# Performance work log

Measured on AMD Instinct MI355X. Metric: run time of the kernel, lower is better.

The kernel has to match this reference:

```python
import jax, jax.numpy as jnp
import numpy as np

DIM = 512; NB = 4; BS = DIM // NB            # EinFFT blocks
DS = 64; DC = 4; EXP = 2; DI = EXP * DIM      # Mamba dims
DTR = DIM // 16                               # dt_rank
BLOCKS = 2; LAM = 0.01; B_SZ = 2; L_SZ = 1024

def layer_norm(x, w, b):
    m = x.mean(-1, keepdims=True)
    v = x.var(-1, keepdims=True)
    return (x - m) / jnp.sqrt(v + 1e-5) * w + b

def softshrink(x, lam):
    return jnp.where(x > lam, x - lam, jnp.where(x < -lam, x + lam, jnp.zeros((), x.dtype)))

def mamba(x, in_proj_w, conv_w, conv_b, x_proj_w, dt_proj_w, dt_proj_b, A_log, D, out_proj_w):
    B, L, _ = x.shape
    xz = x @ in_proj_w.T                      # (B,L,2*DI)
    xm, z = jnp.split(xz, 2, axis=-1)
    # causal depthwise conv1d, keep first L outputs
    xt = xm.transpose(0, 2, 1)                # (B,DI,L)
    conv = jax.lax.conv_general_dilated(xt, conv_w, (1,), [(DC - 1, 0)],
                                        feature_group_count=DI,
                                        dimension_numbers=('NCH', 'OIH', 'NCH'))
    xm = jax.nn.silu((conv + conv_b[None, :, None]).transpose(0, 2, 1))  # (B,L,DI)
    proj = xm @ x_proj_w.T                    # (B,L,DTR+2*DS)
    dt = proj[..., :DTR]
    Bm = proj[..., DTR:DTR + DS]
    Cm = proj[..., DTR + DS:]
    dt = jax.nn.softplus(dt @ dt_proj_w.T + dt_proj_b)   # (B,L,DI)
    A = -jnp.exp(A_log)                       # (DI,DS)

    def step(h, inp):
        dt_t, B_t, C_t, u_t = inp             # (B,DI),(B,DS),(B,DS),(B,DI)
        dA = jnp.exp(dt_t[:, :, None] * A)
        h = dA * h + dt_t[:, :, None] * B_t[:, None, :] * u_t[:, :, None]
        y = jnp.einsum('bds,bs->bd', h, C_t)
        return h, y

    h0 = jnp.zeros((B, DI, DS), x.dtype)
    _, ys = jax.lax.scan(step, h0, (dt.transpose(1, 0, 2), Bm.transpose(1, 0, 2),
                                    Cm.transpose(1, 0, 2), xm.transpose(1, 0, 2)))
    y = ys.transpose(1, 0, 2) + xm * D        # (B,L,DI)
    y = y * jax.nn.silu(z)
    return y @ out_proj_w.T

def einfft(x, cw1, cw2, cb1, cb2):
    B, N, C = x.shape
    xf = jnp.fft.fft2(x.reshape(B, N, NB, BS), axes=(1, 2), norm='ortho')
    mul = lambda t, w: jnp.einsum('BNbd,bdk->BNbk', t, w)
    r1 = jax.nn.relu(mul(xf.real, cw1[0]) - mul(xf.imag, cw1[1]) + cb1[0])
    i1 = jax.nn.relu(mul(xf.real, cw1[1]) + mul(xf.imag, cw1[0]) + cb1[1])
    r2 = softshrink(mul(r1, cw2[0]) - mul(i1, cw2[1]) + cb2[0], LAM)
    i2 = softshrink(mul(r1, cw2[1]) + mul(i1, cw2[0]) + cb2[1], LAM)
    out = jnp.fft.ifft2(r2 + 1j * i2, axes=(1, 2), norm='ortho')
    return out.real.astype(x.dtype).reshape(B, N, C)

def setup_inputs() -> dict:
    key = jax.random.key(0)
    ks = jax.random.split(key, 16)
    r = lambda i, shape, s: jax.random.normal(ks[i], shape, jnp.float32) * s
    A_log = jnp.log(jnp.tile(jnp.arange(1, DS + 1, dtype=jnp.float32), (DI, 1)))
    return {
        'x': jax.random.normal(ks[0], (B_SZ, L_SZ, DIM), jnp.float32),
        'ln_w': jnp.ones((DIM,), jnp.float32), 'ln_b': jnp.zeros((DIM,), jnp.float32),
        'in_proj_w': r(1, (2 * DI, DIM), 0.02),
        'conv_w': r(2, (DI, 1, DC), 0.1), 'conv_b': jnp.zeros((DI,), jnp.float32),
        'x_proj_w': r(3, (DTR + 2 * DS, DI), 0.02),
        'dt_proj_w': r(4, (DI, DTR), 0.02),
        'dt_proj_b': jnp.full((DI,), float(np.log(np.expm1(0.01))), jnp.float32),
        'A_log': A_log, 'D': jnp.ones((DI,), jnp.float32),
        'out_proj_w': r(5, (DIM, DI), 0.02),
        'norm2_w': jnp.ones((DIM,), jnp.float32), 'norm2_b': jnp.zeros((DIM,), jnp.float32),
        'cw1': r(6, (2, NB, BS, BS), 0.02), 'cw2': r(7, (2, NB, BS, BS), 0.02),
        'cb1': r(8, (2, NB, BS), 0.02), 'cb2': r(9, (2, NB, BS), 0.02),
    }

def reference(x, ln_w, ln_b, in_proj_w, conv_w, conv_b, x_proj_w, dt_proj_w, dt_proj_b,
              A_log, D, out_proj_w, norm2_w, norm2_b, cw1, cw2, cb1, cb2):
    for _ in range(BLOCKS):
        x = x + mamba(layer_norm(x, ln_w, ln_b), in_proj_w, conv_w, conv_b,
                      x_proj_w, dt_proj_w, dt_proj_b, A_log, D, out_proj_w)
        x = x + einfft(layer_norm(x, norm2_w, norm2_b), cw1, cw2, cb1, cb2)
    return x
```

## Files before the change

kernel.cpp:

```cpp
#include <hip/hip_runtime.h>

typedef unsigned short u16;
typedef __attribute__((ext_vector_type(8))) short bf8;
typedef __attribute__((ext_vector_type(4))) float f4;

__device__ __forceinline__ float bf2f(u16 b) {
    return __uint_as_float(((unsigned)b) << 16);
}
__device__ __forceinline__ u16 f2bf(float f) {
    unsigned u = __float_as_uint(f);
    u += 0x7fffu + ((u >> 16) & 1u);
    return (u16)(u >> 16);
}
__device__ __forceinline__ void pack8f(const float* v, u16* dst) {
    uint r0 = (uint)f2bf(v[0]) | ((uint)f2bf(v[1]) << 16);
    uint r1 = (uint)f2bf(v[2]) | ((uint)f2bf(v[3]) << 16);
    uint r2 = (uint)f2bf(v[4]) | ((uint)f2bf(v[5]) << 16);
    uint r3 = (uint)f2bf(v[6]) | ((uint)f2bf(v[7]) << 16);
    *(uint4*)dst = make_uint4(r0, r1, r2, r3);
}
__device__ __forceinline__ void pack8u(const u16* v, u16* dst) {
    uint r0 = (uint)v[0] | ((uint)v[1] << 16);
    uint r1 = (uint)v[2] | ((uint)v[3] << 16);
    uint r2 = (uint)v[4] | ((uint)v[5] << 16);
    uint r3 = (uint)v[6] | ((uint)v[7] << 16);
    *(uint4*)dst = make_uint4(r0, r1, r2, r3);
}
__device__ __forceinline__ bf8 neg8(bf8 v) {
    union { bf8 b; uint u[4]; } t; t.b = v;
    t.u[0] ^= 0x80008000u; t.u[1] ^= 0x80008000u;
    t.u[2] ^= 0x80008000u; t.u[3] ^= 0x80008000u;
    return t.b;
}

__global__ void detect_k(const u16* __restrict__ dtb, int* __restrict__ flag) {
    flag[0] = (dtb[0] == dtb[1] && dtb[1] == dtb[2] && dtb[2] == dtb[3] &&
               dtb[3] == dtb[4] && dtb[4] == dtb[5]) ? 1 : 0;
    flag[1] = 1;
}

__global__ __launch_bounds__(256)
void achk_k(const float* __restrict__ alog, int* __restrict__ flag) {
    int i = blockIdx.x * 256 + threadIdx.x;
    int s = i & 63;
    float n = __expf(alog[i]);
    float e = (float)(s + 1);
    if (fabsf(n - e) > 0.02f * e) atomicAnd(&flag[1], 0);
}

struct CvtArgs {
    const void* src[18];
    void* dst[18];
    int n[18];
    int obf[18];
};
__global__ __launch_bounds__(256)
void cvt_all_k(CvtArgs a, const int* __restrict__ flag) {
    const int t = blockIdx.y;
    const int n = a.n[t];
    const int f = flag[0];
    if (a.obf[t]) {
        u16* __restrict__ d = (u16*)a.dst[t];
        if (f) {
            const u16* __restrict__ s = (const u16*)a.src[t];
            for (int i = blockIdx.x * 256 + threadIdx.x; i < n; i += gridDim.x * 256)
                d[i] = s[i];
        } else {
            const float* __restrict__ s = (const float*)a.src[t];
            for (int i = blockIdx.x * 256 + threadIdx.x; i < n; i += gridDim.x * 256)
                d[i] = f2bf(s[i]);
        }
    } else {
        float* __restrict__ d = (float*)a.dst[t];
        if (f) {
            const u16* __restrict__ s = (const u16*)a.src[t];
            for (int i = blockIdx.x * 256 + threadIdx.x; i < n; i += gridDim.x * 256)
                d[i] = bf2f(s[i]);
        } else {
            const float* __restrict__ s = (const float*)a.src[t];
            for (int i = blockIdx.x * 256 + threadIdx.x; i < n; i += gridDim.x * 256)
                d[i] = s[i];
        }
    }
}

__global__ void out_k(const float* __restrict__ in, void* __restrict__ out,
                      int n, const int* __restrict__ flag) {
    int i = blockIdx.x * 256 + threadIdx.x;
    if (i >= n) return;
    if (flag[0]) ((u16*)out)[i] = f2bf(in[i]);
    else         ((float*)out)[i] = in[i];
}

__global__ void wtr_k(const float* __restrict__ src, u16* __restrict__ dst) {
    int idx = blockIdx.x * 256 + threadIdx.x;
    int cin = idx & 127, cout = (idx >> 7) & 127, snb = idx >> 14;
    dst[(snb << 14) + (cout << 7) + cin] = f2bf(src[(snb << 14) + (cin << 7) + cout]);
}

__global__ __launch_bounds__(256)
void ln_k(const float* __restrict__ x, const float* __restrict__ w,
          const float* __restrict__ b, u16* __restrict__ out) {
    const int row = blockIdx.x, tid = threadIdx.x;
    const float* xr = x + (long)row * 512;
    float v0 = xr[tid], v1 = xr[tid + 256];
    float s = v0 + v1, q = v0 * v0 + v1 * v1;
#pragma unroll
    for (int off = 32; off; off >>= 1) {
        s += __shfl_xor(s, off);
        q += __shfl_xor(q, off);
    }
    __shared__ float ss[4], qq[4];
    int wid = tid >> 6;
    if ((tid & 63) == 0) { ss[wid] = s; qq[wid] = q; }
    __syncthreads();
    s = ss[0] + ss[1] + ss[2] + ss[3];
    q = qq[0] + qq[1] + qq[2] + qq[3];
    float mean = s * (1.f / 512.f);
    float var = q * (1.f / 512.f) - mean * mean;
    float rstd = rsqrtf(var + 1e-5f);
    u16* o = out + (long)row * 512;
    o[tid]       = f2bf((v0 - mean) * rstd * w[tid]       + b[tid]);
    o[tid + 256] = f2bf((v1 - mean) * rstd * w[tid + 256] + b[tid + 256]);
}

#define LSTR 40
template <int TAF, int EPI>
__global__ __launch_bounds__(256)
void mgemm_k(const void* __restrict__ Ap, const u16* __restrict__ Bp,
             float* __restrict__ D, int N, int K, int lda, int ldb, int ldc,
             const float* __restrict__ bias, const float* __restrict__ res) {
    const float* Af = (const float*)Ap;
    const u16*  Ab  = (const u16*)Ap;

    __shared__ u16 As[64 * LSTR];
    __shared__ u16 Bs[64 * LSTR];
    const int tid = threadIdx.x;
    const int lane = tid & 63;
    const int w = tid >> 6, wm = w & 1, wn = w >> 1;
    const int m0 = blockIdx.y * 64, n0 = blockIdx.x * 64;
    const int fr = (lane & 15), fq = (lane >> 4);

    f4 acc[2][2] = {};

    for (int k0 = 0; k0 < K; k0 += 32) {
        {
            const int ar = tid >> 2, aks = (tid & 3) << 3;
            if constexpr (TAF) {
                *(uint4*)&As[ar * LSTR + aks] =
                    *(const uint4*)(Ab + (long)(m0 + ar) * lda + k0 + aks);
            } else {
                const float* p = Af + (long)(m0 + ar) * lda + k0 + aks;
                float tv[8];
                float4 x = *(const float4*)p, y = *(const float4*)(p + 4);
                tv[0] = x.x; tv[1] = x.y; tv[2] = x.z; tv[3] = x.w;
                tv[4] = y.x; tv[5] = y.y; tv[6] = y.z; tv[7] = y.w;
                pack8f(tv, &As[ar * LSTR + aks]);
            }
        }
        {
            const int br = tid >> 2, bks = (tid & 3) << 3;
            uint4 raw = make_uint4(0, 0, 0, 0);
            if (n0 + br < N)
                raw = *(const uint4*)(Bp + (long)(n0 + br) * ldb + k0 + bks);
            *(uint4*)&Bs[br * LSTR + bks] = raw;
        }
        __syncthreads();
        bf8 af[2], bff[2];
#pragma unroll
        for (int t = 0; t < 2; t++) {
            af[t]  = *(bf8*)&As[(wm * 32 + t * 16 + fr) * LSTR + (fq << 3)];
            bff[t] = *(bf8*)&Bs[(wn * 32 + t * 16 + fr) * LSTR + (fq << 3)];
        }
#pragma unroll
        for (int i = 0; i < 2; i++)
#pragma unroll
            for (int j = 0; j < 2; j++)
                acc[i][j] = __builtin_amdgcn_mfma_f32_16x16x32_bf16(
                    af[i], bff[j], acc[i][j], 0, 0, 0);
        __syncthreads();
    }

#pragma unroll
    for (int i = 0; i < 2; i++) {
#pragma unroll
        for (int j = 0; j < 2; j++) {
            const int gmb = m0 + wm * 32 + i * 16 + (fq << 2);
            const int gn  = n0 + wn * 32 + j * 16 + fr;
            if (gn >= N) continue;
            float v[4];
#pragma unroll
            for (int e = 0; e < 4; e++) v[e] = acc[i][j][e];
            if constexpr (EPI == 1) {
                float bb = bias[gn];
#pragma unroll
                for (int e = 0; e < 4; e++) {
                    float t = v[e] + bb;
                    v[e] = (t > 20.f) ? t : log1pf(__expf(t));
                }
            }
#pragma unroll
            for (int e = 0; e < 4; e++) {
                long idx = (long)(gmb + e) * ldc + gn;
                float t = v[e];
                if constexpr (EPI == 2) t += res[idx];
                D[idx] = t;
            }
        }
    }
}

__global__ __launch_bounds__(256)
void fftn_k(const u16* __restrict__ xn, float* __restrict__ Xr,
            float* __restrict__ Xi) {
    const int bc = blockIdx.x;
    const int b = bc >> 9, c = bc & 511;
    const int tid = threadIdx.x;
    __shared__ float re[1056], im[1056], twr[512], twi[512];
#pragma unroll
    for (int r = 0; r < 2; ++r) {
        int k = tid + r * 256;
        float s, cc;
        __sincosf((float)k * -6.1359231515425649e-3f, &s, &cc);
        twr[k] = cc; twi[k] = s;
    }
    const u16* src = xn + ((long)b * 1024) * 512 + c;
#pragma unroll
    for (int r = 0; r < 4; ++r) {
        int n = tid + r * 256;
        float v = bf2f(src[(long)n * 512]);
        int a = n + (n >> 5);
        re[a] = v; im[a] = 0.f;
    }
#pragma unroll
    for (int lh = 9; lh >= 0; --lh) {
        __syncthreads();
        const int half = 1 << lh;
#pragma unroll
        for (int r = 0; r < 2; ++r) {
            int j = tid + r * 256;
            int p = j & (half - 1);
            int i0 = ((j >> lh) << (lh + 1)) | p;
            int i1 = i0 + half;
            int a0 = i0 + (i0 >> 5), a1 = i1 + (i1 >> 5);
            float ar = re[a0], ai = im[a0];
            float br = re[a1], bi = im[a1];
            int tn = p << (9 - lh);
            float wr = twr[tn], wi = twi[tn];
            re[a0] = ar + br; im[a0] = ai + bi;
            float tr = ar - br, ti = ai - bi;
            re[a1] = tr * wr - ti * wi;
            im[a1] = tr * wi + ti * wr;
        }
    }
    __syncthreads();
    float* dr = Xr + (long)bc * 1024;
    float* di = Xi + (long)bc * 1024;
#pragma unroll
    for (int r = 0; r < 4; ++r) {
        int kf = tid + r * 256;
        int sidx = __brev((unsigned)kf) >> 22;
        int a = sidx + (sidx >> 5);
        dr[kf] = re[a] * 0.03125f;
        di[kf] = im[a] * 0.03125f;
    }
}

__global__ __launch_bounds__(256)
void ifftn_k(const u16* __restrict__ X2r, const u16* __restrict__ X2i,
             float* __restrict__ Yc) {
    const int bc = blockIdx.x;
    const int tid = threadIdx.x;
    __shared__ float re[1056], im[1056], twr[512], twi[512];
#pragma unroll
    for (int r = 0; r < 2; ++r) {
        int k = tid + r * 256;
        float s, cc;
        __sincosf((float)k * 6.1359231515425649e-3f, &s, &cc);
        twr[k] = cc; twi[k] = s;
    }
    const u16* sr = X2r + (long)bc * 1024;
    const u16* si = X2i + (long)bc * 1024;
    {
        int k4 = tid * 4;
        uint2 pr = *(const uint2*)&sr[k4];
        uint2 pi = *(const uint2*)&si[k4];
        u16 rv[4] = {(u16)(pr.x & 0xFFFF), (u16)(pr.x >> 16),
                     (u16)(pr.y & 0xFFFF), (u16)(pr.y >> 16)};
        u16 iv[4] = {(u16)(pi.x & 0xFFFF), (u16)(pi.x >> 16),
                     (u16)(pi.y & 0xFFFF), (u16)(pi.y >> 16)};
#pragma unroll
        for (int e = 0; e < 4; ++e) {
            int idx = k4 + e;
            int a = idx + (idx >> 5);
            re[a] = bf2f(rv[e]);
            im[a] = bf2f(iv[e]);
        }
    }
#pragma unroll
    for (int lh = 9; lh >= 0; --lh) {
        __syncthreads();
        const int half = 1 << lh;
#pragma unroll
        for (int r = 0; r < 2; ++r) {
            int j = tid + r * 256;
            int p = j & (half - 1);
            int i0 = ((j >> lh) << (lh + 1)) | p;
            int i1 = i0 + half;
            int a0 = i0 + (i0 >> 5), a1 = i1 + (i1 >> 5);
            float ar = re[a0], ai = im[a0];
            float br = re[a1], bi = im[a1];
            int tn = p << (9 - lh);
            float wr = twr[tn], wi = twi[tn];
            re[a0] = ar + br; im[a0] = ai + bi;
            float tr = ar - br, ti = ai - bi;
            re[a1] = tr * wr - ti * wi;
            im[a1] = tr * wi + ti * wr;
        }
    }
    __syncthreads();
    float* d = Yc + (long)bc * 1024;
#pragma unroll
    for (int r = 0; r < 4; ++r) {
        int n = tid + r * 256;
        int sidx = __brev((unsigned)n) >> 22;
        int a = sidx + (sidx >> 5);
        d[n] = re[a] * 0.03125f;
    }
}

__global__ __launch_bounds__(256)
void transadd_k(float* __restrict__ xbuf, const float* __restrict__ Yc) {
    const int b = blockIdx.z;
    const int c0 = blockIdx.x * 64, n0 = blockIdx.y * 64;
    __shared__ float T[64][65];
    const int tid = threadIdx.x;
    const int r = tid >> 2, q = (tid & 3) * 16;
    const float* src = Yc + ((long)(b * 512 + c0 + r)) * 1024 + n0 + q;
#pragma unroll
    for (int k = 0; k < 4; ++k) {
        float4 v = *(const float4*)(src + k * 4);
        T[r][q + k * 4 + 0] = v.x; T[r][q + k * 4 + 1] = v.y;
        T[r][q + k * 4 + 2] = v.z; T[r][q + k * 4 + 3] = v.w;
    }
    __syncthreads();
    float* dst = xbuf + ((long)(b * 1024 + n0 + r)) * 512 + c0 + q;
#pragma unroll
    for (int k = 0; k < 4; ++k) {
        float4 w = *(const float4*)(dst + k * 4);
        w.x += T[q + k * 4 + 0][r]; w.y += T[q + k * 4 + 1][r];
        w.z += T[q + k * 4 + 2][r]; w.w += T[q + k * 4 + 3][r];
        *(float4*)(dst + k * 4) = w;
    }
}

template <int ACT>
__global__ __launch_bounds__(256)
void cmix_k(const u16* __restrict__ Xr, const u16* __restrict__ Xi,
            const u16* __restrict__ WT, const float* __restrict__ cb,
            u16* __restrict__ Or, u16* __restrict__ Oi) {
    const int z = blockIdx.z, b = z >> 2, nb = z & 3;
    const u16* Ar = Xr + (long)b * 524288 + nb * 131072;
    const u16* Ai = Xi + (long)b * 524288 + nb * 131072;
    const u16* Wr = WT + nb * 16384;
    const u16* Wi = WT + 65536 + nb * 16384;
    u16* Dr = Or + (long)b * 524288 + nb * 131072;
    u16* Di = Oi + (long)b * 524288 + nb * 131072;
    __shared__ u16 Ars[64 * LSTR], Ais[64 * LSTR], Brs[64 * LSTR], Bis[64 * LSTR];
    const int tid = threadIdx.x, lane = tid & 63;
    const int w = tid >> 6, wm = w & 1, wn = w >> 1;
    const int m0 = blockIdx.y * 64, n0 = blockIdx.x * 64;
    const int fr = (lane & 15), fq = (lane >> 4);
    f4 accr[2][2] = {}, acci[2][2] = {};

    for (int k0 = 0; k0 < 128; k0 += 32) {
        {
            const int am = tid & 63, akb = (tid >> 6) << 3;
            u16 tr[8], ti[8];
#pragma unroll
            for (int j = 0; j < 8; j++) {
                long off = (long)(k0 + akb + j) * 1024 + m0 + am;
                tr[j] = Ar[off]; ti[j] = Ai[off];
            }
            pack8u(tr, &Ars[am * LSTR + akb]);
            pack8u(ti, &Ais[am * LSTR + akb]);
        }
        {
            const int br = tid >> 2, bks = (tid & 3) << 3;
            *(uint4*)&Brs[br * LSTR + bks] =
                *(const uint4*)(Wr + (long)(n0 + br) * 128 + k0 + bks);
            *(uint4*)&Bis[br * LSTR + bks] =
                *(const uint4*)(Wi + (long)(n0 + br) * 128 + k0 + bks);
        }
        __syncthreads();
        bf8 arf[2], aif[2], brf[2], bif[2];
#pragma unroll
        for (int t = 0; t < 2; t++) {
            arf[t] = *(bf8*)&Ars[(wm * 32 + t * 16 + fr) * LSTR + (fq << 3)];
            aif[t] = *(bf8*)&Ais[(wm * 32 + t * 16 + fr) * LSTR + (fq << 3)];
            brf[t] = *(bf8*)&Brs[(wn * 32 + t * 16 + fr) * LSTR + (fq << 3)];
            bif[t] = *(bf8*)&Bis[(wn * 32 + t * 16 + fr) * LSTR + (fq << 3)];
        }
        bf8 nai[2] = { neg8(aif[0]), neg8(aif[1]) };
#pragma unroll
        for (int i = 0; i < 2; i++)
#pragma unroll
            for (int j = 0; j < 2; j++) {
                accr[i][j] = __builtin_amdgcn_mfma_f32_16x16x32_bf16(arf[i], brf[j], accr[i][j], 0, 0, 0);
                accr[i][j] = __builtin_amdgcn_mfma_f32_16x16x32_bf16(nai[i], bif[j], accr[i][j], 0, 0, 0);
                acci[i][j] = __builtin_amdgcn_mfma_f32_16x16x32_bf16(arf[i], bif[j], acci[i][j], 0, 0, 0);
                acci[i][j] = __builtin_amdgcn_mfma_f32_16x16x32_bf16(aif[i], brf[j], acci[i][j], 0, 0, 0);
            }
        __syncthreads();
    }
#pragma unroll
    for (int i = 0; i < 2; i++)
#pragma unroll
        for (int j = 0; j < 2; j++) {
            const int gmb = m0 + wm * 32 + i * 16 + (fq << 2);
            const int gn  = n0 + wn * 32 + j * 16 + fr;
            const float bbr = cb[nb * 128 + gn];
            const float bbi = cb[512 + nb * 128 + gn];
            u16 pr[4], pi[4];
#pragma unroll
            for (int e = 0; e < 4; e++) {
                float vr = accr[i][j][e] + bbr;
                float vi = acci[i][j][e] + bbi;
                if (ACT == 0) {
                    vr = fmaxf(vr, 0.f);
                    vi = fmaxf(vi, 0.f);
                } else {
                    vr = (vr > 0.01f) ? vr - 0.01f : ((vr < -0.01f) ? vr + 0.01f : 0.f);
                    vi = (vi > 0.01f) ? vi - 0.01f : ((vi < -0.01f) ? vi + 0.01f : 0.f);
                }
                pr[e] = f2bf(vr); pi[e] = f2bf(vi);
            }
            uint2 wr2, wi2;
            wr2.x = (uint)pr[0] | ((uint)pr[1] << 16);
            wr2.y = (uint)pr[2] | ((uint)pr[3] << 16);
            wi2.x = (uint)pi[0] | ((uint)pi[1] << 16);
            wi2.y = (uint)pi[2] | ((uint)pi[3] << 16);
            *(uint2*)&Dr[(long)gn * 1024 + gmb] = wr2;
            *(uint2*)&Di[(long)gn * 1024 + gmb] = wi2;
        }
}

__global__ __launch_bounds__(256)
void conv_k(const float* __restrict__ xz, const float* __restrict__ cw,
            const float* __restrict__ cb, float* __restrict__ u) {
    int idx = blockIdx.x * 256 + threadIdx.x;
    int d = idx & 1023;
    int l = (idx >> 10) & 1023;
    int b = idx >> 20;
    float acc = cb[d];
    const float* base = xz + (long)b * 1024 * 2048 + d;
#pragma unroll
    for (int j = 0; j < 4; j++) {
        int li = l - 3 + j;
        if (li >= 0) acc = fmaf(cw[d * 4 + j], base[(long)li * 2048], acc);
    }
    float sig = 1.f / (1.f + __expf(-acc));
    u[idx] = acc * sig;
}

__global__ __launch_bounds__(256)
void scan1_k(const float* __restrict__ dtL, const float* __restrict__ uL,
             const float* __restrict__ projL, const float* __restrict__ alog,
             u16* __restrict__ Hb, float* __restrict__ Sbuf,
             const int* __restrict__ flag) {
    const int dg = blockIdx.x, c = blockIdx.y, b = blockIdx.z;
    const int tid = threadIdx.x;
    const int d = dg * 256 + tid;
    const int t0 = c * 16;
    __shared__ float Bls[16][64];
    {
        int r = tid >> 4, cg = (tid & 15) << 2;
        *(float4*)&Bls[r][cg] =
            *(const float4*)(projL + ((long)(b * 1024 + t0 + r)) * 160 + 32 + cg);
    }
    __syncthreads();

    float h[64];
#pragma unroll
    for (int s = 0; s < 64; s++) h[s] = 0.f;
    float S = 0.f;
    const float* dtp = dtL + (long)(b * 1024 + t0) * 1024 + d;
    const float* up  = uL  + (long)(b * 1024 + t0) * 1024 + d;

    if (flag[1]) {
        for (int t = 0; t < 16; ++t) {
            float dt = dtp[(long)t * 1024];
            float uu = up[(long)t * 1024];
            float dtu = dt * uu;
            S += dt;
            float q = __expf(-dt);
            float q2 = q * q, q3 = q2 * q, q4 = q2 * q2;
            float a0 = q, a1 = q2, a2 = q3, a3 = q4;
            const float4* B4p = (const float4*)&Bls[t][0];
#pragma unroll
            for (int sg = 0; sg < 16; ++sg) {
                float4 B4 = B4p[sg];
                h[sg * 4 + 0] = a0 * h[sg * 4 + 0] + dtu * B4.x;
                h[sg * 4 + 1] = a1 * h[sg * 4 + 1] + dtu * B4.y;
                h[sg * 4 + 2] = a2 * h[sg * 4 + 2] + dtu * B4.z;
                h[sg * 4 + 3] = a3 * h[sg * 4 + 3] + dtu * B4.w;
                a0 *= q4; a1 *= q4; a2 *= q4; a3 *= q4;
            }
        }
    } else {
        float A[64];
        const float* ap = alog + (long)d * 64;
#pragma unroll
        for (int s = 0; s < 64; s += 4) {
            float4 a4 = *(const float4*)(ap + s);
            A[s] = -__expf(a4.x); A[s + 1] = -__expf(a4.y);
            A[s + 2] = -__expf(a4.z); A[s + 3] = -__expf(a4.w);
        }
        for (int t = 0; t < 16; ++t) {
            float dt = dtp[(long)t * 1024];
            float uu = up[(long)t * 1024];
            float dtu = dt * uu;
            S += dt;
            const float4* B4p = (const float4*)&Bls[t][0];
#pragma unroll
            for (int sg = 0; sg < 16; ++sg) {
                float4 B4 = B4p[sg];
                h[sg * 4 + 0] = __expf(dt * A[sg * 4 + 0]) * h[sg * 4 + 0] + dtu * B4.x;
                h[sg * 4 + 1] = __expf(dt * A[sg * 4 + 1]) * h[sg * 4 + 1] + dtu * B4.y;
                h[sg * 4 + 2] = __expf(dt * A[sg * 4 + 2]) * h[sg * 4 + 2] + dtu * B4.z;
                h[sg * 4 + 3] = __expf(dt * A[sg * 4 + 3]) * h[sg * 4 + 3] + dtu * B4.w;
            }
        }
    }
    u16* Hp = Hb + ((((long)(b * 64 + c)) * 1024 + d) << 6);
#pragma unroll
    for (int s = 0; s < 64; s += 4) {
        uint2 p;
        p.x = ((__float_as_uint(h[s]) + 0x8000u) >> 16) |
              ((__float_as_uint(h[s + 1]) + 0x8000u) & 0xFFFF0000u);
        p.y = ((__float_as_uint(h[s + 2]) + 0x8000u) >> 16) |
              ((__float_as_uint(h[s + 3]) + 0x8000u) & 0xFFFF0000u);
        *(uint2*)&Hp[s] = p;
    }
    Sbuf[(b * 64 + c) * 1024 + d] = S;
}

__global__ __launch_bounds__(256)
void scan2_k(const float* __restrict__ alog, const float* __restrict__ Sbuf,
             u16* __restrict__ Hb) {
    int idx = blockIdx.x * 256 + threadIdx.x;
    int s = idx & 63, d = (idx >> 6) & 1023, b = idx >> 16;
    float A = -__expf(alog[(long)d * 64 + s]);
    float carry = 0.f;
    for (int c = 0; c < 64; ++c) {
        float S = Sbuf[(b * 64 + c) * 1024 + d];
        float P = __expf(A * S);
        long off = ((((long)(b * 64 + c)) * 1024 + d) << 6) + s;
        float H = bf2f(Hb[off]);
        Hb[off] = (u16)((__float_as_uint(carry) + 0x8000u) >> 16);
        carry = P * carry + H;
    }
}

__global__ __launch_bounds__(256)
void scan3_k(float* __restrict__ dtL, const float* __restrict__ uL,
             const float* __restrict__ xz, const float* __restrict__ projL,
             const float* __restrict__ alog, const u16* __restrict__ Hb,
             const float* __restrict__ Dw, const int* __restrict__ flag) {
    const int dg = blockIdx.x, c = blockIdx.y, b = blockIdx.z;
    const int tid = threadIdx.x;
    const int d = dg * 256 + tid;
    const int t0 = c * 16;
    __shared__ float Bls[16][64];
    __shared__ float Cls[16][64];
    {
        int r = tid >> 4, cg = (tid & 15) << 2;
        const float* src = projL + ((long)(b * 1024 + t0 + r)) * 160 + 32 + cg;
        *(float4*)&Bls[r][cg] = *(const float4*)src;
        *(float4*)&Cls[r][cg] = *(const float4*)(src + 64);
    }
    __syncthreads();

    float h[64];
    const u16* Hp = Hb + ((((long)(b * 64 + c)) * 1024 + d) << 6);
#pragma unroll
    for (int s = 0; s < 64; s += 4) {
        uint2 p = *(const uint2*)&Hp[s];
        h[s]     = __uint_as_float(p.x << 16);
        h[s + 1] = __uint_as_float(p.x & 0xFFFF0000u);
        h[s + 2] = __uint_as_float(p.y << 16);
        h[s + 3] = __uint_as_float(p.y & 0xFFFF0000u);
    }
    const float Dd = Dw[d];
    float* dtp = dtL + (long)(b * 1024 + t0) * 1024 + d;
    const float* up = uL + (long)(b * 1024 + t0) * 1024 + d;
    const float* zp = xz + (long)(b * 1024 + t0) * 2048 + 1024 + d;

    if (flag[1]) {
        for (int t = 0; t < 16; ++t) {
            float dt = dtp[(long)t * 1024];
            float uu = up[(long)t * 1024];
            float zz = zp[(long)t * 2048];
            float dtu = dt * uu;
            float y = 0.f;
            float q = __expf(-dt);
            float q2 = q * q, q3 = q2 * q, q4 = q2 * q2;
            float a0 = q, a1 = q2, a2 = q3, a3 = q4;
            const float4* B4p = (const float4*)&Bls[t][0];
            const float4* C4p = (const float4*)&Cls[t][0];
#pragma unroll
            for (int sg = 0; sg < 16; ++sg) {
                float4 B4 = B4p[sg];
                float4 C4 = C4p[sg];
                h[sg * 4 + 0] = a0 * h[sg * 4 + 0] + dtu * B4.x;
                y = fmaf(h[sg * 4 + 0], C4.x, y);
                h[sg * 4 + 1] = a1 * h[sg * 4 + 1] + dtu * B4.y;
                y = fmaf(h[sg * 4 + 1], C4.y, y);
                h[sg * 4 + 2] = a2 * h[sg * 4 + 2] + dtu * B4.z;
                y = fmaf(h[sg * 4 + 2], C4.z, y);
                h[sg * 4 + 3] = a3 * h[sg * 4 + 3] + dtu * B4.w;
                y = fmaf(h[sg * 4 + 3], C4.w, y);
                a0 *= q4; a1 *= q4; a2 *= q4; a3 *= q4;
            }
            float g = zz / (1.f + __expf(-zz));
            dtp[(long)t * 1024] = (y + uu * Dd) * g;
        }
    } else {
        float A[64];
        const float* ap = alog + (long)d * 64;
#pragma unroll
        for (int s = 0; s < 64; s += 4) {
            float4 a4 = *(const float4*)(ap + s);
            A[s] = -__expf(a4.x); A[s + 1] = -__expf(a4.y);
            A[s + 2] = -__expf(a4.z); A[s + 3] = -__expf(a4.w);
        }
        for (int t = 0; t < 16; ++t) {
            float dt = dtp[(long)t * 1024];
            float uu = up[(long)t * 1024];
            float zz = zp[(long)t * 2048];
            float dtu = dt * uu;
            float y = 0.f;
            const float4* B4p = (const float4*)&Bls[t][0];
            const float4* C4p = (const float4*)&Cls[t][0];
#pragma unroll
            for (int sg = 0; sg < 16; ++sg) {
                float4 B4 = B4p[sg];
                float4 C4 = C4p[sg];
                h[sg * 4 + 0] = __expf(dt * A[sg * 4 + 0]) * h[sg * 4 + 0] + dtu * B4.x;
                y = fmaf(h[sg * 4 + 0], C4.x, y);
                h[sg * 4 + 1] = __expf(dt * A[sg * 4 + 1]) * h[sg * 4 + 1] + dtu * B4.y;
                y = fmaf(h[sg * 4 + 1], C4.y, y);
                h[sg * 4 + 2] = __expf(dt * A[sg * 4 + 2]) * h[sg * 4 + 2] + dtu * B4.z;
                y = fmaf(h[sg * 4 + 2], C4.z, y);
                h[sg * 4 + 3] = __expf(dt * A[sg * 4 + 3]) * h[sg * 4 + 3] + dtu * B4.w;
                y = fmaf(h[sg * 4 + 3], C4.w, y);
            }
            float g = zz / (1.f + __expf(-zz));
            dtp[(long)t * 1024] = (y + uu * Dd) * g;
        }
    }
}

__global__ __launch_bounds__(256)
void fft4_k(const float* __restrict__ Xr, const float* __restrict__ Xi,
            u16* __restrict__ Orb, u16* __restrict__ Oib) {
    int idx = blockIdx.x * 256 + threadIdx.x;
    int kf = idx & 1023, c = (idx >> 10) & 127, b = idx >> 17;
    long base = (long)b * 524288 + (long)c * 1024 + kf;
    const int S = 131072;
    float r0 = Xr[base], r1 = Xr[base + S], r2 = Xr[base + 2 * S], r3 = Xr[base + 3 * S];
    float i0 = Xi[base], i1 = Xi[base + S], i2 = Xi[base + 2 * S], i3 = Xi[base + 3 * S];
    Orb[base]         = f2bf((r0 + r1 + r2 + r3) * 0.5f);
    Oib[base]         = f2bf((i0 + i1 + i2 + i3) * 0.5f);
    Orb[base + S]     = f2bf((r0 + i1 - r2 - i3) * 0.5f);
    Oib[base + S]     = f2bf((i0 - r1 - i2 + r3) * 0.5f);
    Orb[base + 2 * S] = f2bf((r0 - r1 + r2 - r3) * 0.5f);
    Oib[base + 2 * S] = f2bf((i0 - i1 + i2 - i3) * 0.5f);
    Orb[base + 3 * S] = f2bf((r0 - i1 - r2 + i3) * 0.5f);
    Oib[base + 3 * S] = f2bf((i0 + r1 - i2 - r3) * 0.5f);
}

__global__ __launch_bounds__(256)
void ifft4_k(u16* __restrict__ Xr, u16* __restrict__ Xi) {
    int idx = blockIdx.x * 256 + threadIdx.x;
    int kf = idx & 1023, c = (idx >> 10) & 127, b = idx >> 17;
    long base = (long)b * 524288 + (long)c * 1024 + kf;
    const int S = 131072;
    float r0 = bf2f(Xr[base]), r1 = bf2f(Xr[base + S]),
          r2 = bf2f(Xr[base + 2 * S]), r3 = bf2f(Xr[base + 3 * S]);
    float i0 = bf2f(Xi[base]), i1 = bf2f(Xi[base + S]),
          i2 = bf2f(Xi[base + 2 * S]), i3 = bf2f(Xi[base + 3 * S]);
    Xr[base]         = f2bf((r0 + r1 + r2 + r3) * 0.5f);
    Xi[base]         = f2bf((i0 + i1 + i2 + i3) * 0.5f);
    Xr[base + S]     = f2bf((r0 - i1 - r2 + i3) * 0.5f);
    Xi[base + S]     = f2bf((i0 + r1 - i2 - r3) * 0.5f);
    Xr[base + 2 * S] = f2bf((r0 - r1 + r2 - r3) * 0.5f);
    Xi[base + 2 * S] = f2bf((i0 - i1 + i2 - i3) * 0.5f);
    Xr[base + 3 * S] = f2bf((r0 + i1 - r2 - i3) * 0.5f);
    Xi[base + 3 * S] = f2bf((i0 - r1 - i2 + r3) * 0.5f);
}

extern "C" void kernel_launch(void* const* d_in, const int* in_sizes, int n_in,
                              void* d_out, int out_size, void* d_ws, size_t ws_size,
                              hipStream_t stream) {
    float* ws = (float*)d_ws;
    int* flag = (int*)ws;
    size_t o = 64;
    float* xbuf  = ws + o; o += 1048576;
    float* xz    = ws + o; o += 4194304;
    float* dtL   = ws + o; o += 2097152;
    float* uL    = ws + o; o += 2097152;
    float* projL = ws + o; o += 327680;
    u16* xnb     = (u16*)(ws + o); o += 524288;
    u16* wInpB   = (u16*)(ws + o); o += 524288;
    u16* wXpB    = (u16*)(ws + o); o += 81920;
    u16* wDtB    = (u16*)(ws + o); o += 16384;
    u16* wOutB   = (u16*)(ws + o); o += 262144;
    u16* WT1     = (u16*)(ws + o); o += 65536;
    u16* WT2     = (u16*)(ws + o); o += 65536;
    float* wCw1f = ws + o; o += 131072;
    float* wCw2f = ws + o; o += 131072;
    float* wConv = ws + o; o += 4096;
    float* wAlog = ws + o; o += 65536;
    float* wLnW  = ws + o; o += 512;
    float* wLnB  = ws + o; o += 512;
    float* wConvB= ws + o; o += 1024;
    float* wDtBias=ws + o; o += 1024;
    float* wD    = ws + o; o += 1024;
    float* wN2w  = ws + o; o += 512;
    float* wN2b  = ws + o; o += 512;
    float* wCb1  = ws + o; o += 1024;
    float* wCb2  = ws + o; o += 1024;
    float* Hreg  = ws + o; o += 4194304;
    float* Sbuf  = ws + o; o += 131072;
    u16* Hb    = (u16*)Hreg;
    float* Xr  = dtL;
    float* Xi  = uL;
    float* Yc  = dtL;
    u16* xzb  = (u16*)xz;
    u16* Xrb  = xzb;
    u16* Xib  = xzb + 1048576;
    u16* r1b  = xzb + 2097152;
    u16* i1b  = xzb + 3145728;
    u16* X2rb = xzb + 4194304;
    u16* X2ib = xzb + 5242880;

    dim3 blk(256);

    detect_k<<<1, 1, 0, stream>>>((const u16*)d_in[8], flag);

    CvtArgs ca;
    void* dsts[18] = {xbuf, wLnW, wLnB, wInpB, wConv, wConvB, wXpB, wDtB, wDtBias,
                      wAlog, wD, wOutB, wN2w, wN2b, wCw1f, wCw2f, wCb1, wCb2};
    int obf[18]    = {0,    0,    0,    1,     0,     0,      1,    1,    0,
                      0,     0,  1,     0,    0,    0,     0,     0,    0};
    for (int i = 0; i < 18; i++) {
        ca.src[i] = d_in[i];
        ca.dst[i] = dsts[i];
        ca.n[i] = in_sizes[i];
        ca.obf[i] = obf[i];
    }
    cvt_all_k<<<dim3(64, 18), blk, 0, stream>>>(ca, flag);
    achk_k<<<256, blk, 0, stream>>>(wAlog, flag);
    wtr_k<<<512, blk, 0, stream>>>(wCw1f, WT1);
    wtr_k<<<512, blk, 0, stream>>>(wCw2f, WT2);

    for (int it = 0; it < 2; ++it) {
        ln_k<<<2048, blk, 0, stream>>>(xbuf, wLnW, wLnB, xnb);
        mgemm_k<1, 0><<<dim3(32, 32), blk, 0, stream>>>(
            xnb, wInpB, xz, 2048, 512, 512, 512, 2048, nullptr, nullptr);
        conv_k<<<8192, blk, 0, stream>>>(xz, wConv, wConvB, uL);
        mgemm_k<0, 0><<<dim3(3, 32), blk, 0, stream>>>(
            uL, wXpB, projL, 160, 1024, 1024, 1024, 160, nullptr, nullptr);
        mgemm_k<0, 1><<<dim3(16, 32), blk, 0, stream>>>(
            projL, wDtB, dtL, 1024, 32, 160, 32, 1024, wDtBias, nullptr);
        scan1_k<<<dim3(4, 64, 2), blk, 0, stream>>>(dtL, uL, projL, wAlog, Hb, Sbuf, flag);
        scan2_k<<<512, blk, 0, stream>>>(wAlog, Sbuf, Hb);
        scan3_k<<<dim3(4, 64, 2), blk, 0, stream>>>(dtL, uL, xz, projL, wAlog, Hb, wD, flag);
        mgemm_k<0, 2><<<dim3(8, 32), blk, 0, stream>>>(
            dtL, wOutB, xbuf, 512, 1024, 1024, 1024, 512, nullptr, xbuf);

        ln_k<<<2048, blk, 0, stream>>>(xbuf, wN2w, wN2b, xnb);
        fftn_k<<<1024, blk, 0, stream>>>(xnb, Xr, Xi);
        fft4_k<<<1024, blk, 0, stream>>>(Xr, Xi, Xrb, Xib);
        cmix_k<0><<<dim3(2, 16, 8), blk, 0, stream>>>(Xrb, Xib, WT1, wCb1, r1b, i1b);
        cmix_k<1><<<dim3(2, 16, 8), blk, 0, stream>>>(r1b, i1b, WT2, wCb2, X2rb, X2ib);
        ifft4_k<<<1024, blk, 0, stream>>>(X2rb, X2ib);
        ifftn_k<<<1024, blk, 0, stream>>>(X2rb, X2ib, Yc);
        transadd_k<<<dim3(8, 16, 2), blk, 0, stream>>>(xbuf, Yc);
    }

    out_k<<<(out_size + 255) / 256, blk, 0, stream>>>(xbuf, d_out, out_size, flag);
}
```

Baseline: 507.3 us.

## Fuse 4-point block FFT into 1024-point FFT kernels and fold weight transpose into conversion

The forward 1024-point FFT and the 4-point FFT across channel blocks are merged into one kernel. Each 1024-thread workgroup handles the four channel blocks of a channel group in shared memory, which removes the fp32 intermediate round trip to global memory and one launch per direction. The inverse path does the same, running the 4-point stage in shared memory before the 1024-point FFT. The EinFFT weight transpose is folded into the input conversion kernel, removing two launches and the fp32 weight staging buffers. The trade-off is a large shared memory footprint and 1024-thread workgroups, with only 256 of them in flight, which may lower occupancy.

```diff
diff --git a/kernel.cpp b/kernel.cpp
--- a/kernel.cpp
+++ b/kernel.cpp
@@ -59,7 +59,23 @@
     const int t = blockIdx.y;
     const int n = a.n[t];
     const int f = flag[0];
-    if (a.obf[t]) {
+    if (a.obf[t] == 2) {
+        u16* __restrict__ d = (u16*)a.dst[t];
+        if (f) {
+            const u16* __restrict__ s = (const u16*)a.src[t];
+            for (int i = blockIdx.x * 256 + threadIdx.x; i < n; i += gridDim.x * 256) {
+                int cin = i & 127, cout = (i >> 7) & 127, snb = i >> 14;
+                d[(snb << 14) + (cout << 7) + cin] = s[(snb << 14) + (cin << 7) + cout];
+            }
+        } else {
+            const float* __restrict__ s = (const float*)a.src[t];
+            for (int i = blockIdx.x * 256 + threadIdx.x; i < n; i += gridDim.x * 256) {
+                int cin = i & 127, cout = (i >> 7) & 127, snb = i >> 14;
+                d[(snb << 14) + (cout << 7) + cin] =
+                    f2bf(s[(snb << 14) + (cin << 7) + cout]);
+            }
+        }
+    } else if (a.obf[t] == 1) {
         u16* __restrict__ d = (u16*)a.dst[t];
         if (f) {
             const u16* __restrict__ s = (const u16*)a.src[t];
@@ -90,12 +106,6 @@
     if (i >= n) return;
     if (flag[0]) ((u16*)out)[i] = f2bf(in[i]);
     else         ((float*)out)[i] = in[i];
-}
-
-__global__ void wtr_k(const float* __restrict__ src, u16* __restrict__ dst) {
-    int idx = blockIdx.x * 256 + threadIdx.x;
-    int cin = idx & 127, cout = (idx >> 7) & 127, snb = idx >> 14;
-    dst[(snb << 14) + (cout << 7) + cin] = f2bf(src[(snb << 14) + (cin << 7) + cout]);
 }
 
 __global__ __launch_bounds__(256)
@@ -210,79 +220,93 @@
     }
 }
 
-__global__ __launch_bounds__(256)
-void fftn_k(const u16* __restrict__ xn, float* __restrict__ Xr,
-            float* __restrict__ Xi) {
-    const int bc = blockIdx.x;
-    const int b = bc >> 9, c = bc & 511;
-    const int tid = threadIdx.x;
-    __shared__ float re[1056], im[1056], twr[512], twi[512];
-#pragma unroll
-    for (int r = 0; r < 2; ++r) {
-        int k = tid + r * 256;
+__global__ __launch_bounds__(1024)
+void ffw_k(const u16* __restrict__ xn, u16* __restrict__ Orb,
+           u16* __restrict__ Oib) {
+    const int bz = blockIdx.x;
+    const int b = bz >> 7, cg = bz & 127;
+    const int t = threadIdx.x;
+    const int f = t >> 8, tl = t & 255;
+    const int c = cg + f * 128;
+    __shared__ float re[4224], im[4224], twr[512], twi[512];
+    if (t < 512) {
         float s, cc;
-        __sincosf((float)k * -6.1359231515425649e-3f, &s, &cc);
-        twr[k] = cc; twi[k] = s;
-    }
+        __sincosf((float)t * -6.1359231515425649e-3f, &s, &cc);
+        twr[t] = cc; twi[t] = s;
+    }
+    float* rf = re + f * 1056;
+    float* mf = im + f * 1056;
     const u16* src = xn + ((long)b * 1024) * 512 + c;
 #pragma unroll
     for (int r = 0; r < 4; ++r) {
-        int n = tid + r * 256;
+        int n = tl + r * 256;
         float v = bf2f(src[(long)n * 512]);
         int a = n + (n >> 5);
-        re[a] = v; im[a] = 0.f;
-    }
+        rf[a] = v; mf[a] = 0.f;
+    }
+    __syncthreads();
 #pragma unroll
     for (int lh = 9; lh >= 0; --lh) {
-        __syncthreads();
         const int half = 1 << lh;
 #pragma unroll
         for (int r = 0; r < 2; ++r) {
-            int j = tid + r * 256;
+            int j = tl + r * 256;
             int p = j & (half - 1);
             int i0 = ((j >> lh) << (lh + 1)) | p;
             int i1 = i0 + half;
             int a0 = i0 + (i0 >> 5), a1 = i1 + (i1 >> 5);
-            float ar = re[a0], ai = im[a0];
-            float br = re[a1], bi = im[a1];
+            float ar = rf[a0], ai = mf[a0];
+            float br = rf[a1], bi = mf[a1];
             int tn = p << (9 - lh);
             float wr = twr[tn], wi = twi[tn];
-            re[a0] = ar + br; im[a0] = ai + bi;
+            rf[a0] = ar + br; mf[a0] = ai + bi;
             float tr = ar - br, ti = ai - bi;
-            re[a1] = tr * wr - ti * wi;
-            im[a1] = tr * wi + ti * wr;
-        }
-    }
-    __syncthreads();
-    float* dr = Xr + (long)bc * 1024;
-    float* di = Xi + (long)bc * 1024;
+            rf[a1] = tr * wr - ti * wi;
+            mf[a1] = tr * wi + ti * wr;
+        }
+        __syncthreads();
+    }
+    u16* dr = Orb + ((long)(b * 512 + c)) * 1024;
+    u16* di = Oib + ((long)(b * 512 + c)) * 1024;
 #pragma unroll
     for (int r = 0; r < 4; ++r) {
-        int kf = tid + r * 256;
+        int kf = tl + r * 256;
         int sidx = __brev((unsigned)kf) >> 22;
         int a = sidx + (sidx >> 5);
-        dr[kf] = re[a] * 0.03125f;
-        di[kf] = im[a] * 0.03125f;
-    }
-}
-
-__global__ __launch_bounds__(256)
-void ifftn_k(const u16* __restrict__ X2r, const u16* __restrict__ X2i,
-             float* __restrict__ Yc) {
-    const int bc = blockIdx.x;
-    const int tid = threadIdx.x;
-    __shared__ float re[1056], im[1056], twr[512], twi[512];
-#pragma unroll
-    for (int r = 0; r < 2; ++r) {
-        int k = tid + r * 256;
+        float r0 = re[a],        i0v = im[a];
+        float r1 = re[1056 + a], i1v = im[1056 + a];
+        float r2 = re[2112 + a], i2v = im[2112 + a];
+        float r3 = re[3168 + a], i3v = im[3168 + a];
+        float vr, vi;
+        if (f == 0)      { vr = r0 + r1 + r2 + r3;     vi = i0v + i1v + i2v + i3v; }
+        else if (f == 1) { vr = r0 + i1v - r2 - i3v;   vi = i0v - r1 - i2v + r3; }
+        else if (f == 2) { vr = r0 - r1 + r2 - r3;     vi = i0v - i1v + i2v - i3v; }
+        else             { vr = r0 - i1v - r2 + i3v;   vi = i0v + r1 - i2v - r3; }
+        dr[kf] = f2bf(vr * 0.015625f);
+        di[kf] = f2bf(vi * 0.015625f);
+    }
+}
+
+__global__ __launch_bounds__(1024)
+void ifw_k(const u16* __restrict__ X2r, const u16* __restrict__ X2i,
+           float* __restrict__ Yc) {
+    const int bz = blockIdx.x;
+    const int b = bz >> 7, cg = bz & 127;
+    const int t = threadIdx.x;
+    const int f = t >> 8, tl = t & 255;
+    const int c = cg + f * 128;
+    __shared__ float re[4224], im[4224], twr[512], twi[512];
+    if (t < 512) {
         float s, cc;
-        __sincosf((float)k * 6.1359231515425649e-3f, &s, &cc);
-        twr[k] = cc; twi[k] = s;
-    }
-    const u16* sr = X2r + (long)bc * 1024;
-    const u16* si = X2i + (long)bc * 1024;
+        __sincosf((float)t * 6.1359231515425649e-3f, &s, &cc);
+        twr[t] = cc; twi[t] = s;
+    }
+    const u16* sr = X2r + ((long)(b * 512 + c)) * 1024;
+    const u16* si = X2i + ((long)(b * 512 + c)) * 1024;
+    float* rf = re + f * 1056;
+    float* mf = im + f * 1056;
+    const int k4 = tl * 4;
     {
-        int k4 = tid * 4;
         uint2 pr = *(const uint2*)&sr[k4];
         uint2 pi = *(const uint2*)&si[k4];
         u16 rv[4] = {(u16)(pr.x & 0xFFFF), (u16)(pr.x >> 16),
@@ -293,39 +317,62 @@
         for (int e = 0; e < 4; ++e) {
             int idx = k4 + e;
             int a = idx + (idx >> 5);
-            re[a] = bf2f(rv[e]);
-            im[a] = bf2f(iv[e]);
-        }
-    }
+            rf[a] = bf2f(rv[e]);
+            mf[a] = bf2f(iv[e]);
+        }
+    }
+    __syncthreads();
+    float vr[4], vi[4];
+#pragma unroll
+    for (int e = 0; e < 4; ++e) {
+        int idx = k4 + e;
+        int a = idx + (idx >> 5);
+        float r0 = re[a],        i0v = im[a];
+        float r1 = re[1056 + a], i1v = im[1056 + a];
+        float r2 = re[2112 + a], i2v = im[2112 + a];
+        float r3 = re[3168 + a], i3v = im[3168 + a];
+        if (f == 0)      { vr[e] = r0 + r1 + r2 + r3;     vi[e] = i0v + i1v + i2v + i3v; }
+        else if (f == 1) { vr[e] = r0 - i1v - r2 + i3v;   vi[e] = i0v + r1 - i2v - r3; }
+        else if (f == 2) { vr[e] = r0 - r1 + r2 - r3;     vi[e] = i0v - i1v + i2v - i3v; }
+        else             { vr[e] = r0 + i1v - r2 - i3v;   vi[e] = i0v - r1 - i2v + r3; }
+        vr[e] *= 0.5f; vi[e] *= 0.5f;
+    }
+    __syncthreads();
+#pragma unroll
+    for (int e = 0; e < 4; ++e) {
+        int idx = k4 + e;
+        int a = idx + (idx >> 5);
+        rf[a] = vr[e]; mf[a] = vi[e];
+    }
+    __syncthreads();
 #pragma unroll
     for (int lh = 9; lh >= 0; --lh) {
-        __syncthreads();
         const int half = 1 << lh;
 #pragma unroll
         for (int r = 0; r < 2; ++r) {
-            int j = tid + r * 256;
+            int j = tl + r * 256;
             int p = j & (half - 1);
             int i0 = ((j >> lh) << (lh + 1)) | p;
             int i1 = i0 + half;
             int a0 = i0 + (i0 >> 5), a1 = i1 + (i1 >> 5);
-            float ar = re[a0], ai = im[a0];
-            float br = re[a1], bi = im[a1];
+            float ar = rf[a0], ai = mf[a0];
+            float br = rf[a1], bi = mf[a1];
             int tn = p << (9 - lh);
             float wr = twr[tn], wi = twi[tn];
-            re[a0] = ar + br; im[a0] = ai + bi;
+            rf[a0] = ar + br; mf[a0] = ai + bi;
             float tr = ar - br, ti = ai - bi;
-            re[a1] = tr * wr - ti * wi;
-            im[a1] = tr * wi + ti * wr;
-        }
-    }
-    __syncthreads();
-    float* d = Yc + (long)bc * 1024;
+            rf[a1] = tr * wr - ti * wi;
+            mf[a1] = tr * wi + ti * wr;
+        }
+        __syncthreads();
+    }
+    float* d = Yc + ((long)(b * 512 + c)) * 1024;
 #pragma unroll
     for (int r = 0; r < 4; ++r) {
-        int n = tid + r * 256;
+        int n = tl + r * 256;
         int sidx = __brev((unsigned)n) >> 22;
         int a = sidx + (sidx >> 5);
-        d[n] = re[a] * 0.03125f;
+        d[n] = rf[a] * 0.03125f;
     }
 }
 
@@ -659,45 +706,6 @@
             dtp[(long)t * 1024] = (y + uu * Dd) * g;
         }
     }
-}
-
-__global__ __launch_bounds__(256)
-void fft4_k(const float* __restrict__ Xr, const float* __restrict__ Xi,
-            u16* __restrict__ Orb, u16* __restrict__ Oib) {
-    int idx = blockIdx.x * 256 + threadIdx.x;
-    int kf = idx & 1023, c = (idx >> 10) & 127, b = idx >> 17;
-    long base = (long)b * 524288 + (long)c * 1024 + kf;
-    const int S = 131072;
-    float r0 = Xr[base], r1 = Xr[base + S], r2 = Xr[base + 2 * S], r3 = Xr[base + 3 * S];
-    float i0 = Xi[base], i1 = Xi[base + S], i2 = Xi[base + 2 * S], i3 = Xi[base + 3 * S];
-    Orb[base]         = f2bf((r0 + r1 + r2 + r3) * 0.5f);
-    Oib[base]         = f2bf((i0 + i1 + i2 + i3) * 0.5f);
-    Orb[base + S]     = f2bf((r0 + i1 - r2 - i3) * 0.5f);
-    Oib[base + S]     = f2bf((i0 - r1 - i2 + r3) * 0.5f);
-    Orb[base + 2 * S] = f2bf((r0 - r1 + r2 - r3) * 0.5f);
-    Oib[base + 2 * S] = f2bf((i0 - i1 + i2 - i3) * 0.5f);
-    Orb[base + 3 * S] = f2bf((r0 - i1 - r2 + i3) * 0.5f);
-    Oib[base + 3 * S] = f2bf((i0 + r1 - i2 - r3) * 0.5f);
-}
-
-__global__ __launch_bounds__(256)
-void ifft4_k(u16* __restrict__ Xr, u16* __restrict__ Xi) {
-    int idx = blockIdx.x * 256 + threadIdx.x;
-    int kf = idx & 1023, c = (idx >> 10) & 127, b = idx >> 17;
-    long base = (long)b * 524288 + (long)c * 1024 + kf;
-    const int S = 131072;
-    float r0 = bf2f(Xr[base]), r1 = bf2f(Xr[base + S]),
-          r2 = bf2f(Xr[base + 2 * S]), r3 = bf2f(Xr[base + 3 * S]);
-    float i0 = bf2f(Xi[base]), i1 = bf2f(Xi[base + S]),
-          i2 = bf2f(Xi[base + 2 * S]), i3 = bf2f(Xi[base + 3 * S]);
-    Xr[base]         = f2bf((r0 + r1 + r2 + r3) * 0.5f);
-    Xi[base]         = f2bf((i0 + i1 + i2 + i3) * 0.5f);
-    Xr[base + S]     = f2bf((r0 - i1 - r2 + i3) * 0.5f);
-    Xi[base + S]     = f2bf((i0 + r1 - i2 - r3) * 0.5f);
-    Xr[base + 2 * S] = f2bf((r0 - r1 + r2 - r3) * 0.5f);
-    Xi[base + 2 * S] = f2bf((i0 - i1 + i2 - i3) * 0.5f);
-    Xr[base + 3 * S] = f2bf((r0 + i1 - r2 - i3) * 0.5f);
-    Xi[base + 3 * S] = f2bf((i0 - r1 - i2 + r3) * 0.5f);
 }
 
 extern "C" void kernel_launch(void* const* d_in, const int* in_sizes, int n_in,
@@ -718,8 +726,6 @@
     u16* wOutB   = (u16*)(ws + o); o += 262144;
     u16* WT1     = (u16*)(ws + o); o += 65536;
     u16* WT2     = (u16*)(ws + o); o += 65536;
-    float* wCw1f = ws + o; o += 131072;
-    float* wCw2f = ws + o; o += 131072;
     float* wConv = ws + o; o += 4096;
     float* wAlog = ws + o; o += 65536;
     float* wLnW  = ws + o; o += 512;
@@ -734,8 +740,6 @@
     float* Hreg  = ws + o; o += 4194304;
     float* Sbuf  = ws + o; o += 131072;
     u16* Hb    = (u16*)Hreg;
-    float* Xr  = dtL;
-    float* Xi  = uL;
     float* Yc  = dtL;
     u16* xzb  = (u16*)xz;
     u16* Xrb  = xzb;
@@ -751,9 +755,9 @@
 
     CvtArgs ca;
     void* dsts[18] = {xbuf, wLnW, wLnB, wInpB, wConv, wConvB, wXpB, wDtB, wDtBias,
-                      wAlog, wD, wOutB, wN2w, wN2b, wCw1f, wCw2f, wCb1, wCb2};
+                      wAlog, wD, wOutB, wN2w, wN2b, WT1, WT2, wCb1, wCb2};
     int obf[18]    = {0,    0,    0,    1,     0,     0,      1,    1,    0,
-                      0,     0,  1,     0,    0,    0,     0,     0,    0};
+                      0,     0,  1,     0,    0,    2,   2,   0,    0};
     for (int i = 0; i < 18; i++) {
         ca.src[i] = d_in[i];
         ca.dst[i] = dsts[i];
@@ -762,8 +766,6 @@
     }
     cvt_all_k<<<dim3(64, 18), blk, 0, stream>>>(ca, flag);
     achk_k<<<256, blk, 0, stream>>>(wAlog, flag);
-    wtr_k<<<512, blk, 0, stream>>>(wCw1f, WT1);
-    wtr_k<<<512, blk, 0, stream>>>(wCw2f, WT2);
 
     for (int it = 0; it < 2; ++it) {
         ln_k<<<2048, blk, 0, stream>>>(xbuf, wLnW, wLnB, xnb);
@@ -781,12 +783,10 @@
             dtL, wOutB, xbuf, 512, 1024, 1024, 1024, 512, nullptr, xbuf);
 
         ln_k<<<2048, blk, 0, stream>>>(xbuf, wN2w, wN2b, xnb);
-        fftn_k<<<1024, blk, 0, stream>>>(xnb, Xr, Xi);
-        fft4_k<<<1024, blk, 0, stream>>>(Xr, Xi, Xrb, Xib);
+        ffw_k<<<256, dim3(1024), 0, stream>>>(xnb, Xrb, Xib);
         cmix_k<0><<<dim3(2, 16, 8), blk, 0, stream>>>(Xrb, Xib, WT1, wCb1, r1b, i1b);
         cmix_k<1><<<dim3(2, 16, 8), blk, 0, stream>>>(r1b, i1b, WT2, wCb2, X2rb, X2ib);
-        ifft4_k<<<1024, blk, 0, stream>>>(X2rb, X2ib);
-        ifftn_k<<<1024, blk, 0, stream>>>(X2rb, X2ib, Yc);
+        ifw_k<<<256, dim3(1024), 0, stream>>>(X2rb, X2ib, Yc);
         transadd_k<<<dim3(8, 16, 2), blk, 0, stream>>>(xbuf, Yc);
     }
 
```

Result: no change. 501.1 us (-1.2%).
